# Performance work log

Measured on AMD Instinct MI355X. Metric: run time of the kernel, lower is better.

Reference implementation:

```python
import jax, jax.numpy as jnp
import numpy as np

# (cin, cout, k, stride, out_hw) for blocks b1..b4 of BlockNet
CFG = [(3, 4, 5, 3, 20), (4, 6, 3, 2, 9), (6, 16, 3, 2, 4), (16, 32, 3, 2, 1)]
BATCH = 2048


def setup_inputs() -> dict:
    key = jax.random.key(0)
    ks = iter(jax.random.split(key, 40))
    d = {"x": jax.random.normal(next(ks), (BATCH, 3, 64, 64), jnp.float32)}
    for i, (cin, cout, k, s, oh) in enumerate(CFG, start=1):
        L = oh * oh
        ln = cin * k * k
        fan = 1.0 / np.sqrt(ln)
        d[f"w_uc{i}"] = jax.random.normal(next(ks), (ln * L, cout), jnp.float32) * fan
        d[f"b_uc{i}"] = jax.random.normal(next(ks), (1, cout, oh, oh), jnp.float32) * 0.02
        d[f"w_pc{i}"] = jax.random.normal(next(ks), (cout, cin, k, k), jnp.float32) * fan
        d[f"b_pc{i}"] = jnp.zeros((cout,), jnp.float32)
        d[f"w_wl{i}"] = jax.random.normal(next(ks), (1, cin, k, k), jnp.float32) * fan
        d[f"b_wl{i}"] = jnp.zeros((1,), jnp.float32)
    d["fc_w"] = jax.random.normal(next(ks), (32, 4), jnp.float32) * (1.0 / np.sqrt(32))
    d["fc_b"] = jnp.zeros((4,), jnp.float32)
    return d


def _unfold(x, k, s):
    # torch.nn.Unfold semantics (VALID, square kernel/stride), feature dim ordered (C, kh, kw)
    B, C, H, W = x.shape
    oh = (H - k) // s + 1
    idx = jnp.arange(oh)[:, None] * s + jnp.arange(k)[None, :]  # [oh, k]
    # patches: [B, C, oh, ow, kh, kw]
    p = x[:, :, idx[:, None, :, None], idx[None, :, None, :]]
    return p.transpose(0, 2, 3, 1, 4, 5).reshape(B, oh * oh, C * k * k), oh


def _conv(x, w, b, s):
    y = jax.lax.conv_general_dilated(x, w, (s, s), 'VALID',
                                     dimension_numbers=('NCHW', 'OIHW', 'NCHW'))
    return y + b[None, :, None, None]


def _block(x, wu, bu, wp, bp, wl, bl, k, s):
    # UntiedConv: the repeat+block-diag-mask+matmul is exactly a per-location matmul:
    # out[b,l,o] = sum_k patches[b,l,k] * wu[l*len+k, o]
    patches, oh = _unfold(x, k, s)           # [B, L, len]
    B, L, ln = patches.shape
    Wl = wu.reshape(L, ln, -1)               # [L, len, cout]
    x1 = jnp.einsum('blk,lko->blo', patches, Wl)
    x1 = x1.transpose(0, 2, 1).reshape(B, -1, oh, oh) + bu
    x2 = _conv(x, wp, bp, s)                 # shared-weight conv path
    g = jax.nn.sigmoid(_conv(x, wl, bl, s))  # per-location gate
    return x1 * g + x2 * (1.0 - g)


def reference(x,
              w_uc1, b_uc1, w_pc1, b_pc1, w_wl1, b_wl1,
              w_uc2, b_uc2, w_pc2, b_pc2, w_wl2, b_wl2,
              w_uc3, b_uc3, w_pc3, b_pc3, w_wl3, b_wl3,
              w_uc4, b_uc4, w_pc4, b_pc4, w_wl4, b_wl4,
              fc_w, fc_b):
    h = jax.nn.relu(_block(x, w_uc1, b_uc1, w_pc1, b_pc1, w_wl1, b_wl1, 5, 3))
    h = jax.nn.relu(_block(h, w_uc2, b_uc2, w_pc2, b_pc2, w_wl2, b_wl2, 3, 2))
    h = jax.nn.relu(_block(h, w_uc3, b_uc3, w_pc3, b_pc3, w_wl3, b_wl3, 3, 2))
    h = jax.nn.relu(_block(h, w_uc4, b_uc4, w_pc4, b_pc4, w_wl4, b_wl4, 3, 2))
    h = h.reshape(h.shape[0], 32)
    return h @ fc_w + fc_b
```

## Files before the change

### kernel.cpp

```cpp
#include <hip/hip_runtime.h>
#include <math.h>


__device__ __forceinline__ float sigmoidf_(float x) {
    return 1.0f / (1.0f + expf(-x));
}

__global__ __launch_bounds__(128)
void block1_fused9(const float* __restrict__ x,
                   const float* __restrict__ w_uc,
                   const float* __restrict__ b_uc,
                   const float* __restrict__ w_pc,
                   const float* __restrict__ b_pc,
                   const float* __restrict__ w_wl,
                   const float* __restrict__ b_wl,
                   float* __restrict__ y1t,
                   int B)
{
    __shared__ __align__(16) float wu_s[1500];
    __shared__ __align__(16) float wp_s[300];
    __shared__ float wl_s[75];
    __shared__ __align__(16) float4 red4[12 * 64];

    const int tid  = threadIdx.x;
    const int lane = tid & 63;
    const int wv   = __builtin_amdgcn_readfirstlane(tid >> 6);
    const int b0   = blockIdx.x * 64;
    const int i    = blockIdx.y >> 2;
    const int jgroup = blockIdx.y & 3;

    {
        const float4* src = reinterpret_cast<const float4*>(w_uc)
                          + (size_t)(i * 20 + jgroup * 5) * 75;
        float4* dst = reinterpret_cast<float4*>(wu_s);
        for (int idx = tid; idx < 375; idx += 128) dst[idx] = src[idx];
        for (int idx = tid; idx < 300; idx += 128)
            wp_s[idx] = w_pc[(idx & 3) * 75 + (idx >> 2)];
        for (int idx = tid; idx < 75; idx += 128) wl_s[idx] = w_wl[idx];
    }
    __syncthreads();

    float au[4][5], ap[4][5], ag[5];
    #pragma unroll
    for (int o = 0; o < 4; ++o)
        #pragma unroll
        for (int jj = 0; jj < 5; ++jj) { au[o][jj] = 0.f; ap[o][jj] = 0.f; }
    #pragma unroll
    for (int jj = 0; jj < 5; ++jj) ag[jj] = 0.f;

    const int col0 = (jgroup == 0) ? 0 : (jgroup == 1) ? 12
                   : (jgroup == 2) ? 28 : 44;
    const int off  = jgroup * 15 - col0;
    const float* xb = x + (size_t)(b0 + lane) * 12288 + (size_t)(i * 3) * 64 + col0;

    const int p0   = wv ? 8 : 0;
    const int pend = wv ? 15 : 8;

    float4 cur[5], nxt[5];
    {
        const int c0 = p0 / 5, a0 = p0 - c0 * 5;
        const float* s0 = xb + c0 * 4096 + a0 * 64;
        #pragma unroll
        for (int q = 0; q < 5; ++q)
            cur[q] = *reinterpret_cast<const float4*>(s0 + q * 4);
    }

    #pragma unroll 1
    for (int p = p0; p < pend; ++p) {
        if (p + 1 < pend) {
            const int pn = p + 1;
            const int cn = pn / 5;
            const int an = pn - cn * 5;
            const float* src = xb + cn * 4096 + an * 64;
            #pragma unroll
            for (int q = 0; q < 5; ++q)
                nxt[q] = *reinterpret_cast<const float4*>(src + q * 4);
        }

        float cf[20];
        #pragma unroll
        for (int q = 0; q < 5; ++q) {
            cf[4 * q + 0] = cur[q].x; cf[4 * q + 1] = cur[q].y;
            cf[4 * q + 2] = cur[q].z; cf[4 * q + 3] = cur[q].w;
        }
        float xv[17];
        if (off == 0) {
            #pragma unroll
            for (int t = 0; t < 17; ++t) xv[t] = cf[t];
        } else if (off == 1) {
            #pragma unroll
            for (int t = 0; t < 17; ++t) xv[t] = cf[t + 1];
        } else if (off == 2) {
            #pragma unroll
            for (int t = 0; t < 17; ++t) xv[t] = cf[t + 2];
        } else {
            #pragma unroll
            for (int t = 0; t < 17; ++t) xv[t] = cf[t + 3];
        }

        const int n0 = p * 5;
        #pragma unroll
        for (int b2 = 0; b2 < 5; ++b2) {
            const float  wlv = wl_s[n0 + b2];
            const float4 wp4 = *reinterpret_cast<const float4*>(&wp_s[(n0 + b2) * 4]);
            #pragma unroll
            for (int jj = 0; jj < 5; ++jj) {
                const float v = xv[3 * jj + b2];
                const float4 w4 = *reinterpret_cast<const float4*>(
                    &wu_s[(jj * 75 + n0 + b2) * 4]);
                ag[jj]    += v * wlv;
                au[0][jj] += v * w4.x;  au[1][jj] += v * w4.y;
                au[2][jj] += v * w4.z;  au[3][jj] += v * w4.w;
                ap[0][jj] += v * wp4.x; ap[1][jj] += v * wp4.y;
                ap[2][jj] += v * wp4.z; ap[3][jj] += v * wp4.w;
            }
        }

        if (p + 1 < pend) {
            #pragma unroll
            for (int q = 0; q < 5; ++q) cur[q] = nxt[q];
        }
    }

    if (wv == 1) {
        #pragma unroll
        for (int jj = 0; jj < 5; ++jj) {
            red4[jj * 64 + lane] =
                make_float4(au[0][jj], au[1][jj], au[2][jj], au[3][jj]);
            red4[(5 + jj) * 64 + lane] =
                make_float4(ap[0][jj], ap[1][jj], ap[2][jj], ap[3][jj]);
        }
        red4[10 * 64 + lane] = make_float4(ag[0], ag[1], ag[2], ag[3]);
        red4[11 * 64 + lane] = make_float4(ag[4], 0.f, 0.f, 0.f);
    }
    __syncthreads();
    if (wv == 0) {
        #pragma unroll
        for (int jj = 0; jj < 5; ++jj) {
            const float4 tu = red4[jj * 64 + lane];
            au[0][jj] += tu.x; au[1][jj] += tu.y;
            au[2][jj] += tu.z; au[3][jj] += tu.w;
            const float4 tp = red4[(5 + jj) * 64 + lane];
            ap[0][jj] += tp.x; ap[1][jj] += tp.y;
            ap[2][jj] += tp.z; ap[3][jj] += tp.w;
        }
        const float4 tg = red4[10 * 64 + lane];
        ag[0] += tg.x; ag[1] += tg.y; ag[2] += tg.z; ag[3] += tg.w;
        ag[4] += red4[11 * 64 + lane].x;

        const float bwl = b_wl[0];
        #pragma unroll
        for (int jj = 0; jj < 5; ++jj) {
            const int l = i * 20 + jgroup * 5 + jj;
            const float g = sigmoidf_(ag[jj] + bwl);
            #pragma unroll
            for (int o = 0; o < 4; ++o) {
                const float x1 = au[o][jj] + b_uc[o * 400 + l];
                const float x2 = ap[o][jj] + b_pc[o];
                y1t[(size_t)(o * 400 + l) * B + b0 + lane] =
                    fmaxf(x1 * g + x2 * (1.f - g), 0.f);
            }
        }
    }
}

template<int CIN, int COUT, int K, int S, int OH, int IH, int VB>
__global__ __launch_bounds__(256)
void blockT_kernel(const float* __restrict__ in_t,
                   const float* __restrict__ w_uc,
                   const float* __restrict__ b_uc,
                   const float* __restrict__ w_pc,
                   const float* __restrict__ b_pc,
                   const float* __restrict__ w_wl,
                   const float* __restrict__ b_wl,
                   float* __restrict__ out_t,
                   int B)
{
    constexpr int LN = CIN * K * K;
    constexpr int L  = OH * OH;
    const int wv   = threadIdx.x >> 6;
    const int lane = threadIdx.x & 63;
    const int l    = __builtin_amdgcn_readfirstlane(blockIdx.y * 4 + wv);
    if (l >= L) return;
    const int i = l / OH, j = l % OH;
    const int b = blockIdx.x * (64 * VB) + lane * VB;

    float au[COUT][VB], ap[COUT][VB], ag[VB];
    #pragma unroll
    for (int o = 0; o < COUT; ++o)
        #pragma unroll
        for (int q = 0; q < VB; ++q) { au[o][q] = 0.f; ap[o][q] = 0.f; }
    #pragma unroll
    for (int q = 0; q < VB; ++q) ag[q] = 0.f;

    const float* wu = w_uc + (size_t)l * LN * COUT;

    #pragma unroll
    for (int c = 0; c < CIN; ++c)
    #pragma unroll
    for (int a = 0; a < K; ++a)
    #pragma unroll
    for (int b2 = 0; b2 < K; ++b2) {
        const int n = c * K * K + a * K + b2;
        const int p = c * IH * IH + (i * S + a) * IH + (j * S + b2);
        float v[VB];
        const float* src = in_t + (size_t)p * B + b;
        if constexpr (VB == 4) {
            const float4 t = *reinterpret_cast<const float4*>(src);
            v[0] = t.x; v[1] = t.y; v[2] = t.z; v[3] = t.w;
        } else if constexpr (VB == 2) {
            const float2 t = *reinterpret_cast<const float2*>(src);
            v[0] = t.x; v[1] = t.y;
        } else {
            v[0] = src[0];
        }
        const float wl = w_wl[n];
        #pragma unroll
        for (int q = 0; q < VB; ++q) ag[q] += v[q] * wl;
        #pragma unroll
        for (int o = 0; o < COUT; ++o) {
            const float wuv = wu[n * COUT + o];
            const float wpv = w_pc[o * LN + n];
            #pragma unroll
            for (int q = 0; q < VB; ++q) {
                au[o][q] += v[q] * wuv;
                ap[o][q] += v[q] * wpv;
            }
        }
    }

    const float bwl = b_wl[0];
    float g[VB];
    #pragma unroll
    for (int q = 0; q < VB; ++q) g[q] = sigmoidf_(ag[q] + bwl);

    #pragma unroll
    for (int o = 0; o < COUT; ++o) {
        const float buc = b_uc[o * L + l];
        const float bpc = b_pc[o];
        float y[VB];
        #pragma unroll
        for (int q = 0; q < VB; ++q) {
            const float x1 = au[o][q] + buc;
            const float x2 = ap[o][q] + bpc;
            y[q] = fmaxf(x1 * g[q] + x2 * (1.f - g[q]), 0.f);
        }
        float* dst = out_t + (size_t)(o * L + l) * B + b;
        if constexpr (VB == 4) {
            float4 t; t.x = y[0]; t.y = y[1]; t.z = y[2]; t.w = y[3];
            *reinterpret_cast<float4*>(dst) = t;
        } else if constexpr (VB == 2) {
            float2 t; t.x = y[0]; t.y = y[1];
            *reinterpret_cast<float2*>(dst) = t;
        } else {
            dst[0] = y[0];
        }
    }
}

__global__ __launch_bounds__(256)
void block4T_fc(const float* __restrict__ in_t,
                const float* __restrict__ w_uc,
                const float* __restrict__ b_uc,
                const float* __restrict__ w_pc,
                const float* __restrict__ b_pc,
                const float* __restrict__ w_wl,
                const float* __restrict__ b_wl,
                const float* __restrict__ fc_w,
                const float* __restrict__ fc_b,
                float* __restrict__ out,
                int B)
{
    __shared__ __align__(16) float wu_s[144 * 36];
    __shared__ __align__(16) float wp_s[144 * 36];
    __shared__ float wl_s[144];
    __shared__ float buc_s[32], bpc_s[32], fcw_s[128], fcb_s[4];
    __shared__ float red[4][64][5];

    const int tid  = threadIdx.x;
    const int wv   = tid >> 6;
    const int lane = tid & 63;
    const int o0   = __builtin_amdgcn_readfirstlane(wv * 8);
    const int b    = blockIdx.x * 64 + lane;

    for (int idx = tid; idx < 144 * 32; idx += 256) {
        wu_s[(idx >> 5) * 36 + (idx & 31)] = w_uc[idx];
        const int o = idx / 144, n = idx - o * 144;
        wp_s[n * 36 + o] = w_pc[idx];
    }
    if (tid < 144) wl_s[tid] = w_wl[tid];
    if (tid < 32)  { buc_s[tid] = b_uc[tid]; bpc_s[tid] = b_pc[tid]; }
    if (tid >= 64 && tid < 192) fcw_s[tid - 64] = fc_w[tid - 64];
    if (tid >= 192 && tid < 196) fcb_s[tid - 192] = fc_b[tid - 192];
    __syncthreads();

    float au[8], apc[8], ag = 0.f;
    #pragma unroll
    for (int oo = 0; oo < 8; ++oo) { au[oo] = 0.f; apc[oo] = 0.f; }

    #pragma unroll
    for (int c = 0; c < 16; ++c) {
        float v[9];
        #pragma unroll
        for (int a = 0; a < 3; ++a)
        #pragma unroll
        for (int b2 = 0; b2 < 3; ++b2)
            v[a * 3 + b2] = in_t[(size_t)(c * 16 + a * 4 + b2) * B + b];

        #pragma unroll
        for (int t = 0; t < 9; ++t) {
            const int n = c * 9 + t;
            ag += v[t] * wl_s[n];
            const float4 wuA = *reinterpret_cast<const float4*>(&wu_s[n * 36 + o0]);
            const float4 wuB = *reinterpret_cast<const float4*>(&wu_s[n * 36 + o0 + 4]);
            const float4 wpA = *reinterpret_cast<const float4*>(&wp_s[n * 36 + o0]);
            const float4 wpB = *reinterpret_cast<const float4*>(&wp_s[n * 36 + o0 + 4]);
            au[0] += v[t] * wuA.x;  au[1] += v[t] * wuA.y;
            au[2] += v[t] * wuA.z;  au[3] += v[t] * wuA.w;
            au[4] += v[t] * wuB.x;  au[5] += v[t] * wuB.y;
            au[6] += v[t] * wuB.z;  au[7] += v[t] * wuB.w;
            apc[0] += v[t] * wpA.x; apc[1] += v[t] * wpA.y;
            apc[2] += v[t] * wpA.z; apc[3] += v[t] * wpA.w;
            apc[4] += v[t] * wpB.x; apc[5] += v[t] * wpB.y;
            apc[6] += v[t] * wpB.z; apc[7] += v[t] * wpB.w;
        }
    }

    const float g = sigmoidf_(ag + b_wl[0]);
    float pf[4] = {0.f, 0.f, 0.f, 0.f};
    #pragma unroll
    for (int oo = 0; oo < 8; ++oo) {
        const int o = o0 + oo;
        const float h = fmaxf((au[oo] + buc_s[o]) * g +
                              (apc[oo] + bpc_s[o]) * (1.f - g), 0.f);
        #pragma unroll
        for (int f = 0; f < 4; ++f) pf[f] += h * fcw_s[o * 4 + f];
    }
    #pragma unroll
    for (int f = 0; f < 4; ++f) red[wv][lane][f] = pf[f];
    __syncthreads();
    if (wv == 0) {
        float4 s;
        s.x = fcb_s[0] + red[0][lane][0] + red[1][lane][0] + red[2][lane][0] + red[3][lane][0];
        s.y = fcb_s[1] + red[0][lane][1] + red[1][lane][1] + red[2][lane][1] + red[3][lane][1];
        s.z = fcb_s[2] + red[0][lane][2] + red[1][lane][2] + red[2][lane][2] + red[3][lane][2];
        s.w = fcb_s[3] + red[0][lane][3] + red[1][lane][3] + red[2][lane][3] + red[3][lane][3];
        *reinterpret_cast<float4*>(out + (size_t)b * 4) = s;
    }
}

template<int CIN, int COUT, int K, int S, int OH, int IH, int BPB>
__global__ __launch_bounds__(256)
void block_kernel(const float* __restrict__ in,
                  const float* __restrict__ w_uc,
                  const float* __restrict__ b_uc,
                  const float* __restrict__ w_pc,
                  const float* __restrict__ b_pc,
                  const float* __restrict__ w_wl,
                  const float* __restrict__ b_wl,
                  float* __restrict__ out,
                  int B)
{
    constexpr int LN   = CIN * K * K;
    constexpr int L    = OH * OH;
    constexpr int TILE = CIN * IH * IH;
    __shared__ __align__(16) float lds[BPB * TILE];

    const int b0 = blockIdx.x * BPB;
    const int nb = (B - b0 < BPB) ? (B - b0) : BPB;
    const int tot = nb * TILE;
    const float* src = in + (size_t)b0 * TILE;
    if ((tot & 3) == 0) {
        const float4* s4 = reinterpret_cast<const float4*>(src);
        float4* d4 = reinterpret_cast<float4*>(lds);
        for (int idx = threadIdx.x; idx < (tot >> 2); idx += blockDim.x) d4[idx] = s4[idx];
    } else {
        for (int idx = threadIdx.x; idx < tot; idx += blockDim.x) lds[idx] = src[idx];
    }
    __syncthreads();

    const float bwl = b_wl[0];
    for (int t = threadIdx.x; t < nb * L; t += blockDim.x) {
        const int bb = t / L;
        const int l  = t % L;
        const int i  = l / OH, j = l % OH;
        const float* tile = lds + bb * TILE;

        float acc_uc[COUT], acc_pc[COUT];
        #pragma unroll
        for (int o = 0; o < COUT; ++o) { acc_uc[o] = 0.f; acc_pc[o] = 0.f; }
        float acc_g = 0.f;

        const float* wu = w_uc + (size_t)l * LN * COUT;
        #pragma unroll
        for (int c = 0; c < CIN; ++c)
        #pragma unroll
        for (int a = 0; a < K; ++a)
        #pragma unroll
        for (int b2 = 0; b2 < K; ++b2) {
            const int n = c * K * K + a * K + b2;
            const float v = tile[c * IH * IH + (i * S + a) * IH + (j * S + b2)];
            acc_g += v * w_wl[n];
            #pragma unroll
            for (int o = 0; o < COUT; ++o) acc_uc[o] += v * wu[n * COUT + o];
            #pragma unroll
            for (int o = 0; o < COUT; ++o) acc_pc[o] += v * w_pc[o * LN + n];
        }

        const float g = sigmoidf_(acc_g + bwl);
        const size_t ob = (size_t)(b0 + bb) * COUT * L;
        #pragma unroll
        for (int o = 0; o < COUT; ++o) {
            const float x1 = acc_uc[o] + b_uc[o * L + l];
            const float x2 = acc_pc[o] + b_pc[o];
            out[ob + o * L + l] = fmaxf(x1 * g + x2 * (1.f - g), 0.f);
        }
    }
}

__global__ __launch_bounds__(256)
void block4_fc_kernel(const float* __restrict__ in,
                      const float* __restrict__ w_uc,
                      const float* __restrict__ b_uc,
                      const float* __restrict__ w_pc,
                      const float* __restrict__ b_pc,
                      const float* __restrict__ w_wl,
                      const float* __restrict__ b_wl,
                      const float* __restrict__ fc_w,
                      const float* __restrict__ fc_b,
                      float* __restrict__ out,
                      int B)
{
    __shared__ float hbuf[8][32];
    const int bl = threadIdx.x >> 5;
    const int o  = threadIdx.x & 31;
    const int b  = blockIdx.x * 8 + bl;

    if (b < B) {
        const float* xb = in + (size_t)b * 256;
        float acc_uc = 0.f, acc_pc = 0.f, acc_g = 0.f;
        #pragma unroll
        for (int c = 0; c < 16; ++c)
        #pragma unroll
        for (int a = 0; a < 3; ++a)
        #pragma unroll
        for (int b2 = 0; b2 < 3; ++b2) {
            const int n = c * 9 + a * 3 + b2;
            const float v = xb[c * 16 + a * 4 + b2];
            acc_uc += v * w_uc[n * 32 + o];
            acc_pc += v * w_pc[o * 144 + n];
            acc_g  += v * w_wl[n];
        }
        const float g  = sigmoidf_(acc_g + b_wl[0]);
        hbuf[bl][o] = fmaxf((acc_uc + b_uc[o]) * g + (acc_pc + b_pc[o]) * (1.f - g), 0.f);
    }
    __syncthreads();

    if (threadIdx.x < 32) {
        const int bl2 = threadIdx.x >> 2;
        const int f   = threadIdx.x & 3;
        const int bb  = blockIdx.x * 8 + bl2;
        if (bb < B) {
            float s = fc_b[f];
            #pragma unroll
            for (int oo = 0; oo < 32; ++oo) s += hbuf[bl2][oo] * fc_w[oo * 4 + f];
            out[(size_t)bb * 4 + f] = s;
        }
    }
}

extern "C" void kernel_launch(void* const* d_in, const int* in_sizes, int n_in,
                              void* d_out, int out_size, void* d_ws, size_t ws_size,
                              hipStream_t stream) {
    const float* x    = (const float*)d_in[0];
    const float* wuc1 = (const float*)d_in[1];
    const float* buc1 = (const float*)d_in[2];
    const float* wpc1 = (const float*)d_in[3];
    const float* bpc1 = (const float*)d_in[4];
    const float* wwl1 = (const float*)d_in[5];
    const float* bwl1 = (const float*)d_in[6];
    const float* wuc2 = (const float*)d_in[7];
    const float* buc2 = (const float*)d_in[8];
    const float* wpc2 = (const float*)d_in[9];
    const float* bpc2 = (const float*)d_in[10];
    const float* wwl2 = (const float*)d_in[11];
    const float* bwl2 = (const float*)d_in[12];
    const float* wuc3 = (const float*)d_in[13];
    const float* buc3 = (const float*)d_in[14];
    const float* wpc3 = (const float*)d_in[15];
    const float* bpc3 = (const float*)d_in[16];
    const float* wwl3 = (const float*)d_in[17];
    const float* bwl3 = (const float*)d_in[18];
    const float* wuc4 = (const float*)d_in[19];
    const float* buc4 = (const float*)d_in[20];
    const float* wpc4 = (const float*)d_in[21];
    const float* bpc4 = (const float*)d_in[22];
    const float* wwl4 = (const float*)d_in[23];
    const float* bwl4 = (const float*)d_in[24];
    const float* fcw  = (const float*)d_in[25];
    const float* fcb  = (const float*)d_in[26];

    const int B = in_sizes[0] / (3 * 64 * 64);
    float* ws = (float*)d_ws;
    const size_t need = sizeof(float) * (size_t)(1600 + 486 + 256) * B;

    if (ws_size >= need && (B % 256) == 0) {
        float* y1 = ws;
        float* y2 = y1 + (size_t)1600 * B;
        float* y3 = y2 + (size_t)486 * B;

        block1_fused9<<<dim3(B / 64, 80), 128, 0, stream>>>(
            x, wuc1, buc1, wpc1, bpc1, wwl1, bwl1, y1, B);
        blockT_kernel<4, 6, 3, 2, 9, 20, 2>
            <<<dim3(B / 128, 21), 256, 0, stream>>>(y1, wuc2, buc2, wpc2, bpc2, wwl2, bwl2, y2, B);
        blockT_kernel<6, 16, 3, 2, 4, 9, 1>
            <<<dim3(B / 64, 4), 256, 0, stream>>>(y2, wuc3, buc3, wpc3, bpc3, wwl3, bwl3, y3, B);
        block4T_fc<<<B / 64, 256, 0, stream>>>(y3, wuc4, buc4, wpc4, bpc4, wwl4, bwl4,
                                               fcw, fcb, (float*)d_out, B);
    } else {
        float* y1 = ws;
        float* y2 = y1 + (size_t)B * 4 * 400;
        float* y3 = y2 + (size_t)B * 6 * 81;
        block_kernel<3, 4, 5, 3, 20, 64, 1>
            <<<B, 256, 0, stream>>>(x, wuc1, buc1, wpc1, bpc1, wwl1, bwl1, y1, B);
        block_kernel<4, 6, 3, 2, 9, 20, 4>
            <<<(B + 3) / 4, 256, 0, stream>>>(y1, wuc2, buc2, wpc2, bpc2, wwl2, bwl2, y2, B);
        block_kernel<6, 16, 3, 2, 4, 9, 16>
            <<<(B + 15) / 16, 256, 0, stream>>>(y2, wuc3, buc3, wpc3, bpc3, wwl3, bwl3, y3, B);
        block4_fc_kernel<<<(B + 7) / 8, 256, 0, stream>>>(
            y3, wuc4, buc4, wpc4, bpc4, wwl4, bwl4, fcw, fcb, (float*)d_out, B);
    }
}
```

Baseline: 97.57 us.

## Split block1 input channels across three waves with all loads issued upfront

The first-block kernel now uses 192 threads, one wave per input channel, in place of two waves splitting 15 kernel rows. Each wave loads its whole 5x5 row window into registers before the barrier, so global loads overlap the weight staging in shared memory. This removes the serial prefetch loop. Partial sums from two waves are reduced through a doubled shared buffer. The cost is more registers per thread (25 float4), which may lower occupancy, plus a larger reduction.

```diff
diff --git a/kernel.cpp b/kernel.cpp
--- a/kernel.cpp
+++ b/kernel.cpp
@@ -6,21 +6,21 @@
     return 1.0f / (1.0f + expf(-x));
 }
 
-__global__ __launch_bounds__(128)
-void block1_fused9(const float* __restrict__ x,
-                   const float* __restrict__ w_uc,
-                   const float* __restrict__ b_uc,
-                   const float* __restrict__ w_pc,
-                   const float* __restrict__ b_pc,
-                   const float* __restrict__ w_wl,
-                   const float* __restrict__ b_wl,
-                   float* __restrict__ y1t,
-                   int B)
+__global__ __launch_bounds__(192)
+void block1_fused10(const float* __restrict__ x,
+                    const float* __restrict__ w_uc,
+                    const float* __restrict__ b_uc,
+                    const float* __restrict__ w_pc,
+                    const float* __restrict__ b_pc,
+                    const float* __restrict__ w_wl,
+                    const float* __restrict__ b_wl,
+                    float* __restrict__ y1t,
+                    int B)
 {
     __shared__ __align__(16) float wu_s[1500];
     __shared__ __align__(16) float wp_s[300];
     __shared__ float wl_s[75];
-    __shared__ __align__(16) float4 red4[12 * 64];
+    __shared__ __align__(16) float4 red4[2][12 * 64];
 
     const int tid  = threadIdx.x;
     const int lane = tid & 63;
@@ -33,55 +33,42 @@
         const float4* src = reinterpret_cast<const float4*>(w_uc)
                           + (size_t)(i * 20 + jgroup * 5) * 75;
         float4* dst = reinterpret_cast<float4*>(wu_s);
-        for (int idx = tid; idx < 375; idx += 128) dst[idx] = src[idx];
-        for (int idx = tid; idx < 300; idx += 128)
+        for (int idx = tid; idx < 375; idx += 192) dst[idx] = src[idx];
+        for (int idx = tid; idx < 300; idx += 192)
             wp_s[idx] = w_pc[(idx & 3) * 75 + (idx >> 2)];
-        for (int idx = tid; idx < 75; idx += 128) wl_s[idx] = w_wl[idx];
-    }
-    __syncthreads();
-
-    float au[4][5], ap[4][5], ag[5];
-    #pragma unroll
-    for (int o = 0; o < 4; ++o)
-        #pragma unroll
-        for (int jj = 0; jj < 5; ++jj) { au[o][jj] = 0.f; ap[o][jj] = 0.f; }
-    #pragma unroll
-    for (int jj = 0; jj < 5; ++jj) ag[jj] = 0.f;
+        for (int idx = tid; idx < 75; idx += 192) wl_s[idx] = w_wl[idx];
+    }
 
     const int col0 = (jgroup == 0) ? 0 : (jgroup == 1) ? 12
                    : (jgroup == 2) ? 28 : 44;
     const int off  = jgroup * 15 - col0;
-    const float* xb = x + (size_t)(b0 + lane) * 12288 + (size_t)(i * 3) * 64 + col0;
-
-    const int p0   = wv ? 8 : 0;
-    const int pend = wv ? 15 : 8;
-
-    float4 cur[5], nxt[5];
-    {
-        const int c0 = p0 / 5, a0 = p0 - c0 * 5;
-        const float* s0 = xb + c0 * 4096 + a0 * 64;
+    const float* xc = x + (size_t)(b0 + lane) * 12288 + (size_t)wv * 4096
+                    + (size_t)(i * 3) * 64 + col0;
+
+    float4 xr[5][5];
+    #pragma unroll
+    for (int k = 0; k < 5; ++k)
         #pragma unroll
         for (int q = 0; q < 5; ++q)
-            cur[q] = *reinterpret_cast<const float4*>(s0 + q * 4);
-    }
-
-    #pragma unroll 1
-    for (int p = p0; p < pend; ++p) {
-        if (p + 1 < pend) {
-            const int pn = p + 1;
-            const int cn = pn / 5;
-            const int an = pn - cn * 5;
-            const float* src = xb + cn * 4096 + an * 64;
-            #pragma unroll
-            for (int q = 0; q < 5; ++q)
-                nxt[q] = *reinterpret_cast<const float4*>(src + q * 4);
-        }
-
+            xr[k][q] = *reinterpret_cast<const float4*>(xc + k * 64 + q * 4);
+
+    __syncthreads();
+
+    float au[4][5], ap[4][5], ag[5];
+    #pragma unroll
+    for (int o = 0; o < 4; ++o)
+        #pragma unroll
+        for (int jj = 0; jj < 5; ++jj) { au[o][jj] = 0.f; ap[o][jj] = 0.f; }
+    #pragma unroll
+    for (int jj = 0; jj < 5; ++jj) ag[jj] = 0.f;
+
+    #pragma unroll
+    for (int k = 0; k < 5; ++k) {
         float cf[20];
         #pragma unroll
         for (int q = 0; q < 5; ++q) {
-            cf[4 * q + 0] = cur[q].x; cf[4 * q + 1] = cur[q].y;
-            cf[4 * q + 2] = cur[q].z; cf[4 * q + 3] = cur[q].w;
+            cf[4 * q + 0] = xr[k][q].x; cf[4 * q + 1] = xr[k][q].y;
+            cf[4 * q + 2] = xr[k][q].z; cf[4 * q + 3] = xr[k][q].w;
         }
         float xv[17];
         if (off == 0) {
@@ -98,7 +85,7 @@
             for (int t = 0; t < 17; ++t) xv[t] = cf[t + 3];
         }
 
-        const int n0 = p * 5;
+        const int n0 = wv * 25 + k * 5;
         #pragma unroll
         for (int b2 = 0; b2 < 5; ++b2) {
             const float  wlv = wl_s[n0 + b2];
@@ -115,38 +102,38 @@
                 ap[2][jj] += v * wp4.z; ap[3][jj] += v * wp4.w;
             }
         }
-
-        if (p + 1 < pend) {
-            #pragma unroll
-            for (int q = 0; q < 5; ++q) cur[q] = nxt[q];
-        }
-    }
-
-    if (wv == 1) {
+    }
+
+    if (wv >= 1) {
+        float4* rb = red4[wv - 1];
         #pragma unroll
         for (int jj = 0; jj < 5; ++jj) {
-            red4[jj * 64 + lane] =
+            rb[jj * 64 + lane] =
                 make_float4(au[0][jj], au[1][jj], au[2][jj], au[3][jj]);
-            red4[(5 + jj) * 64 + lane] =
+            rb[(5 + jj) * 64 + lane] =
                 make_float4(ap[0][jj], ap[1][jj], ap[2][jj], ap[3][jj]);
         }
-        red4[10 * 64 + lane] = make_float4(ag[0], ag[1], ag[2], ag[3]);
-        red4[11 * 64 + lane] = make_float4(ag[4], 0.f, 0.f, 0.f);
+        rb[10 * 64 + lane] = make_float4(ag[0], ag[1], ag[2], ag[3]);
+        rb[11 * 64 + lane] = make_float4(ag[4], 0.f, 0.f, 0.f);
     }
     __syncthreads();
     if (wv == 0) {
         #pragma unroll
-        for (int jj = 0; jj < 5; ++jj) {
-            const float4 tu = red4[jj * 64 + lane];
-            au[0][jj] += tu.x; au[1][jj] += tu.y;
-            au[2][jj] += tu.z; au[3][jj] += tu.w;
-            const float4 tp = red4[(5 + jj) * 64 + lane];
-            ap[0][jj] += tp.x; ap[1][jj] += tp.y;
-            ap[2][jj] += tp.z; ap[3][jj] += tp.w;
-        }
-        const float4 tg = red4[10 * 64 + lane];
-        ag[0] += tg.x; ag[1] += tg.y; ag[2] += tg.z; ag[3] += tg.w;
-        ag[4] += red4[11 * 64 + lane].x;
+        for (int w2 = 0; w2 < 2; ++w2) {
+            const float4* rb = red4[w2];
+            #pragma unroll
+            for (int jj = 0; jj < 5; ++jj) {
+                const float4 tu = rb[jj * 64 + lane];
+                au[0][jj] += tu.x; au[1][jj] += tu.y;
+                au[2][jj] += tu.z; au[3][jj] += tu.w;
+                const float4 tp = rb[(5 + jj) * 64 + lane];
+                ap[0][jj] += tp.x; ap[1][jj] += tp.y;
+                ap[2][jj] += tp.z; ap[3][jj] += tp.w;
+            }
+            const float4 tg = rb[10 * 64 + lane];
+            ag[0] += tg.x; ag[1] += tg.y; ag[2] += tg.z; ag[3] += tg.w;
+            ag[4] += rb[11 * 64 + lane].x;
+        }
 
         const float bwl = b_wl[0];
         #pragma unroll
@@ -509,7 +496,7 @@
         float* y2 = y1 + (size_t)1600 * B;
         float* y3 = y2 + (size_t)486 * B;
 
-        block1_fused9<<<dim3(B / 64, 80), 128, 0, stream>>>(
+        block1_fused10<<<dim3(B / 64, 80), 192, 0, stream>>>(
             x, wuc1, buc1, wpc1, bpc1, wwl1, bwl1, y1, B);
         blockT_kernel<4, 6, 3, 2, 9, 20, 2>
             <<<dim3(B / 128, 21), 256, 0, stream>>>(y1, wuc2, buc2, wpc2, bpc2, wwl2, bwl2, y2, B);
```

Result: slower. 200.2 us (+105.2%).

## Split block3 input channels across waves and halve block2 batch per thread

Applied to the files above, without the earlier changes.

Adds a dedicated block-3 kernel where each pair of waves splits the six input channels in halves for one output location. The partial sums for the untied conv, the shared conv and the gate are combined through shared memory before the epilogue. The block-2 launch now uses one batch element per thread with twice the grid in x. Both changes aim to expose more parallelism and shorten per-thread serial work at batch 2048, at the cost of an extra reduction and barrier and of weights read directly from global memory instead of staged.

```diff
diff --git a/kernel.cpp b/kernel.cpp
--- a/kernel.cpp
+++ b/kernel.cpp
@@ -254,6 +254,84 @@
             *reinterpret_cast<float2*>(dst) = t;
         } else {
             dst[0] = y[0];
+        }
+    }
+}
+
+__global__ __launch_bounds__(256)
+void block3T_split(const float* __restrict__ in_t,
+                   const float* __restrict__ w_uc,
+                   const float* __restrict__ b_uc,
+                   const float* __restrict__ w_pc,
+                   const float* __restrict__ b_pc,
+                   const float* __restrict__ w_wl,
+                   const float* __restrict__ b_wl,
+                   float* __restrict__ out_t,
+                   int B)
+{
+    __shared__ __align__(16) float4 red4[2][9][64];
+
+    const int tid   = threadIdx.x;
+    const int lane  = tid & 63;
+    const int w     = __builtin_amdgcn_readfirstlane(tid >> 6);
+    const int lslot = w >> 1;
+    const int chalf = w & 1;
+    const int l     = blockIdx.y * 2 + lslot;
+    const int i     = l >> 2, j = l & 3;
+    const int b     = blockIdx.x * 64 + lane;
+
+    float au[16], ap[16], ag = 0.f;
+    #pragma unroll
+    for (int o = 0; o < 16; ++o) { au[o] = 0.f; ap[o] = 0.f; }
+
+    const float* wu = w_uc + (size_t)l * 54 * 16;
+    #pragma unroll
+    for (int cc = 0; cc < 3; ++cc) {
+        const int c = chalf * 3 + cc;
+        #pragma unroll
+        for (int a = 0; a < 3; ++a)
+        #pragma unroll
+        for (int b2 = 0; b2 < 3; ++b2) {
+            const int n = c * 9 + a * 3 + b2;
+            const int p = c * 81 + (i * 2 + a) * 9 + (j * 2 + b2);
+            const float v = in_t[(size_t)p * B + b];
+            ag += v * w_wl[n];
+            #pragma unroll
+            for (int o = 0; o < 16; ++o) {
+                au[o] += v * wu[n * 16 + o];
+                ap[o] += v * w_pc[o * 54 + n];
+            }
+        }
+    }
+
+    if (chalf == 1) {
+        #pragma unroll
+        for (int q = 0; q < 4; ++q) {
+            red4[lslot][q][lane] =
+                make_float4(au[4*q], au[4*q+1], au[4*q+2], au[4*q+3]);
+            red4[lslot][4 + q][lane] =
+                make_float4(ap[4*q], ap[4*q+1], ap[4*q+2], ap[4*q+3]);
+        }
+        red4[lslot][8][lane] = make_float4(ag, 0.f, 0.f, 0.f);
+    }
+    __syncthreads();
+    if (chalf == 0) {
+        #pragma unroll
+        for (int q = 0; q < 4; ++q) {
+            const float4 tu = red4[lslot][q][lane];
+            au[4*q] += tu.x; au[4*q+1] += tu.y; au[4*q+2] += tu.z; au[4*q+3] += tu.w;
+            const float4 tp = red4[lslot][4 + q][lane];
+            ap[4*q] += tp.x; ap[4*q+1] += tp.y; ap[4*q+2] += tp.z; ap[4*q+3] += tp.w;
+        }
+        ag += red4[lslot][8][lane].x;
+
+        const float g = sigmoidf_(ag + b_wl[0]);
+        #pragma unroll
+        for (int o = 0; o < 16; ++o) {
+            const float x1 = au[o] + b_uc[o * 16 + l];
+            const float x2 = ap[o] + b_pc[o];
+            out_t[(size_t)(o * 16 + l) * B + b] =
+                fmaxf(x1 * g + x2 * (1.f - g), 0.f);
         }
     }
 }
@@ -511,10 +589,10 @@
 
         block1_fused9<<<dim3(B / 64, 80), 128, 0, stream>>>(
             x, wuc1, buc1, wpc1, bpc1, wwl1, bwl1, y1, B);
-        blockT_kernel<4, 6, 3, 2, 9, 20, 2>
-            <<<dim3(B / 128, 21), 256, 0, stream>>>(y1, wuc2, buc2, wpc2, bpc2, wwl2, bwl2, y2, B);
-        blockT_kernel<6, 16, 3, 2, 4, 9, 1>
-            <<<dim3(B / 64, 4), 256, 0, stream>>>(y2, wuc3, buc3, wpc3, bpc3, wwl3, bwl3, y3, B);
+        blockT_kernel<4, 6, 3, 2, 9, 20, 1>
+            <<<dim3(B / 64, 21), 256, 0, stream>>>(y1, wuc2, buc2, wpc2, bpc2, wwl2, bwl2, y2, B);
+        block3T_split<<<dim3(B / 64, 8), 256, 0, stream>>>(
+            y2, wuc3, buc3, wpc3, bpc3, wwl3, bwl3, y3, B);
         block4T_fc<<<B / 64, 256, 0, stream>>>(y3, wuc4, buc4, wpc4, bpc4, wwl4, bwl4,
                                                fcw, fcb, (float*)d_out, B);
     } else {
```

Result: faster. 78.77 us (median of 2 runs) (-19.3%).
